# Kernel optimization log

Hardware: AMD Instinct MI355X
Metric: run time of the kernel (lower is better)

Reference implementation:

```python
import jax, jax.numpy as jnp
import numpy as np


def setup_inputs() -> dict:
    key = jax.random.key(0)
    k1, k2 = jax.random.split(key)
    x = jax.random.normal(k1, (32, 64, 64, 64), dtype=jnp.float32)
    codebook = jax.random.normal(k2, (1024, 64), dtype=jnp.float32)
    return {"x": x, "codebook": codebook}


def reference(x, codebook):
    # x: (B, D, H, W)  codebook: (K, D)
    B, D = x.shape[0], x.shape[1]
    spatial = x.shape[2:]
    flat = x.reshape(B, D, -1).transpose(0, 2, 1)  # (B, N, D)
    dot = jnp.einsum("bnd,kd->bnk", flat, codebook)
    cb_norm = jnp.sum(codebook * codebook, axis=-1)  # (K,)
    indices = jnp.argmin(cb_norm[None, None, :] - 2.0 * dot, axis=-1)  # (B, N)
    quantized = codebook[indices]  # (B, N, D) gather
    out = quantized.transpose(0, 2, 1).reshape(x.shape)
    return out, indices.reshape((B,) + spatial)
```

## Files before the change

kernel.cpp:

```cpp
#include <hip/hip_runtime.h>


typedef _Float16 f16x8 __attribute__((ext_vector_type(8)));
typedef float    f32x4 __attribute__((ext_vector_type(4)));

#define VQ_D    64
#define VQ_HW   4096
#define VQ_NPOS 131072
#define SC      2048.0f
#define EPS_Q   24
#define WS_CBN  65536
#define WS_CNQ  66560
#define WS_CBT  67584

__global__ __launch_bounds__(256)
void vq_prep(const float* __restrict__ cb, float* __restrict__ ws)
{
    const int tid = threadIdx.x;
    const int blk = blockIdx.x;
    if (blk < 64) {
        const int it   = blk * 256 + tid;
        const int ct   = it >> 8;
        const int s    = (it >> 6) & 3;
        const int lane = it & 63;
        const int ks   = s & 1, isR = s >> 1;
        const int n    = ct * 16 + (lane & 15);
        const int k0   = ks * 32 + (lane >> 4) * 8;
        const float* src = cb + n * 64 + k0;
        f16x8 o;
        #pragma unroll
        for (int j = 0; j < 8; ++j) {
            const float b = src[j];
            const _Float16 bh = (_Float16)b;
            o[j] = isR ? (_Float16)((b - (float)bh) * (-2.0f * SC))
                       : (_Float16)(-2.0f * (float)bh);
        }
        ((f16x8*)ws)[it] = o;
    } else if (blk < 128) {
        const int it = (blk - 64) * 256 + tid;
        const int k = it >> 4, j4 = it & 15;
        ((float4*)(ws + WS_CBT))[j4 * 1024 + k] = ((const float4*)cb)[it];
    } else {
        const int k = (blk - 128) * 256 + tid;
        const float4* row = (const float4*)(cb + k * 64);
        float a0 = 0.f, a1 = 0.f, a2 = 0.f, a3 = 0.f;
        #pragma unroll
        for (int j = 0; j < 16; ++j) {
            const float4 c = row[j];
            a0 = fmaf(c.x, c.x, a0); a1 = fmaf(c.y, c.y, a1);
            a2 = fmaf(c.z, c.z, a2); a3 = fmaf(c.w, c.w, a3);
        }
        const float cn = (a0 + a1) + (a2 + a3);
        ws[WS_CBN + k] = cn;
        ws[WS_CNQ + k] = cn * 2048.0f;
    }
}

#define GLOAD_LDS(GP, LP)                                                     \
    __builtin_amdgcn_global_load_lds(                                         \
        (const __attribute__((address_space(1))) unsigned int*)(GP),          \
        (__attribute__((address_space(3))) unsigned int*)(LP), 16, 0, 0)

#define STAGE2(CK, BOFF)                                                      \
    {                                                                         \
        const char* gs_ = (const char*)ws + (size_t)(CK) * 8192               \
                          + wv * 2048 + lane * 16;                            \
        char* ld_ = (char*)bbuf + (BOFF) + wv * 2048;                         \
        GLOAD_LDS(gs_, ld_);                                                  \
        GLOAD_LDS(gs_ + 1024, ld_ + 1024);                                    \
    }

#define CT_BODY(BOFF, CI, CTG)                                                \
    {                                                                         \
        const f16x8 B0 = *(const f16x8*)(lp + (BOFF) + (CI) * 4096);          \
        const f16x8 B1 = *(const f16x8*)(lp + (BOFF) + (CI) * 4096 + 1024);   \
        const f16x8 R0 = *(const f16x8*)(lp + (BOFF) + (CI) * 4096 + 2048);   \
        const f16x8 R1 = *(const f16x8*)(lp + (BOFF) + (CI) * 4096 + 3072);   \
        const float cvq = cnq_lds[(CTG) * 16 + m];                            \
        const f32x4 Ci = {cvq, cvq, cvq, cvq};                                \
        f32x4 pa[4], pb[4];                                                   \
        __builtin_amdgcn_s_setprio(1);                                        \
        _Pragma("unroll")                                                     \
        for (int tl = 0; tl < 4; ++tl) {                                      \
            pa[tl] = __builtin_amdgcn_mfma_f32_16x16x32_f16(Ak[tl][0], B0, Ci,    0,0,0); \
            pb[tl] = __builtin_amdgcn_mfma_f32_16x16x32_f16(Ak[tl][1], B1, zero4, 0,0,0); \
        }                                                                     \
        _Pragma("unroll")                                                     \
        for (int tl = 0; tl < 4; ++tl) {                                      \
            pa[tl] = __builtin_amdgcn_mfma_f32_16x16x32_f16(Ah[tl][0], R0, pa[tl], 0,0,0); \
            pb[tl] = __builtin_amdgcn_mfma_f32_16x16x32_f16(Ah[tl][1], R1, pb[tl], 0,0,0); \
        }                                                                     \
        _Pragma("unroll")                                                     \
        for (int tl = 0; tl < 4; ++tl) {                                      \
            pa[tl] = __builtin_amdgcn_mfma_f32_16x16x32_f16(Ra[tl][0], B0, pa[tl], 0,0,0); \
            pb[tl] = __builtin_amdgcn_mfma_f32_16x16x32_f16(Ra[tl][1], B1, pb[tl], 0,0,0); \
        }                                                                     \
        __builtin_amdgcn_s_setprio(0);                                        \
        const int cbase_ = (CTG) * 16 + m;                                    \
        _Pragma("unroll")                                                     \
        for (int tl = 0; tl < 4; ++tl)                                        \
            _Pragma("unroll")                                                 \
            for (int r = 0; r < 4; ++r) {                                     \
                const float q_ = pa[tl][r] + pb[tl][r];                       \
                const int k_ = ((int)q_ << 10) | cbase_;                      \
                int md_;                                                      \
                asm("v_med3_i32 %0, %1, %2, %3"                               \
                    : "=v"(md_) : "v"(k_), "v"(d1[tl][r]), "v"(d2[tl][r]));   \
                d2[tl][r] = md_;                                              \
                d1[tl][r] = (k_ < d1[tl][r]) ? k_ : d1[tl][r];                \
            }                                                                 \
    }

#define ITER_T(VMSTR, DOSTAGE, T)                                             \
    {                                                                         \
        asm volatile("s_waitcnt " VMSTR ::: "memory");                        \
        __builtin_amdgcn_s_barrier();                                         \
        if (DOSTAGE) STAGE2((T) + 3, (((T) + 3) & 3) * 8192)                  \
        const int base_ = ((T) & 3) * 8192;                                   \
        CT_BODY(base_, 0, (T) * 2)                                            \
        CT_BODY(base_, 1, (T) * 2 + 1)                                        \
    }

__global__ __launch_bounds__(256, 2)
void vq_main(const float* __restrict__ x,
             const float* __restrict__ cb,
             float* __restrict__ ws,
             float* __restrict__ out,
             float* __restrict__ idx_out)
{
    __shared__ f16x8 bbuf[4 * 512];
    __shared__ float cnq_lds[1024];
    __shared__ int   sk[256];
    __shared__ int   smg[256];
    __shared__ int   lpos[256];
    __shared__ int   lcnt;

    const int tid  = threadIdx.x;
    const int lane = tid & 63;
    const int wv   = tid >> 6;
    const int m    = lane & 15;
    const int q    = lane >> 4;

    const int p0 = blockIdx.x * 256;
    const int b  = p0 >> 12;
    const int n0 = p0 & (VQ_HW - 1);
    const float* xw = x + (size_t)b * (VQ_D * VQ_HW) + n0 + wv * 64;

    STAGE2(0, 0)
    STAGE2(1, 8192)
    STAGE2(2, 16384)

    ((float4*)cnq_lds)[tid] = ((const float4*)(ws + WS_CNQ))[tid];

    f16x8 Ah[4][2], Ak[4][2], Ra[4][2];
    #pragma unroll
    for (int tl = 0; tl < 4; ++tl)
        #pragma unroll
        for (int ks = 0; ks < 2; ++ks) {
            f16x8 h8, k8, r8;
            #pragma unroll
            for (int j = 0; j < 8; ++j) {
                const float v = xw[(size_t)(ks * 32 + q * 8 + j) * VQ_HW + tl * 16 + m];
                const _Float16 vh = (_Float16)v;
                h8[j] = vh;
                k8[j] = (_Float16)((float)vh * 2048.0f);
                r8[j] = (_Float16)((v - (float)vh) * SC);
            }
            Ah[tl][ks] = h8; Ak[tl][ks] = k8; Ra[tl][ks] = r8;
        }

    int d1[4][4], d2[4][4];
    #pragma unroll
    for (int tl = 0; tl < 4; ++tl)
        #pragma unroll
        for (int r = 0; r < 4; ++r) { d1[tl][r] = 0x7FFFFFFF; d2[tl][r] = 0x7FFFFFFF; }

    const f32x4 zero4 = {0.f, 0.f, 0.f, 0.f};
    const char* lp = (const char*)bbuf + lane * 16;

    __syncthreads();

    for (int t = 0; t < 29; ++t)
        ITER_T("vmcnt(4)", 1, t)
    ITER_T("vmcnt(4)", 0, 29)
    ITER_T("vmcnt(2)", 0, 30)
    ITER_T("vmcnt(0)", 0, 31)

    #pragma unroll
    for (int off = 1; off < 16; off <<= 1)
        #pragma unroll
        for (int tl = 0; tl < 4; ++tl)
            #pragma unroll
            for (int r = 0; r < 4; ++r) {
                const int od1 = __shfl_xor(d1[tl][r], off, 64);
                const int od2 = __shfl_xor(d2[tl][r], off, 64);
                const int mx  = (d1[tl][r] > od1) ? d1[tl][r] : od1;
                const int mn2 = (d2[tl][r] < od2) ? d2[tl][r] : od2;
                d2[tl][r] = (mx < mn2) ? mx : mn2;
                d1[tl][r] = (d1[tl][r] < od1) ? d1[tl][r] : od1;
            }

    if (m == 0) {
        #pragma unroll
        for (int tl = 0; tl < 4; ++tl)
            #pragma unroll
            for (int r = 0; r < 4; ++r) {
                const int li = wv * 64 + tl * 16 + q * 4 + r;
                sk[li]  = d1[tl][r] & 1023;
                smg[li] = (d2[tl][r] >> 10) - (d1[tl][r] >> 10);
            }
    }
    if (tid == 0) lcnt = 0;
    __syncthreads();

    const int bk = sk[tid];
    idx_out[p0 + tid] = (float)bk;
    {
        const float4* cr = (const float4*)(cb + (size_t)bk * VQ_D);
        float* ob = out + (size_t)b * (VQ_D * VQ_HW) + n0 + tid;
        #pragma unroll
        for (int d4 = 0; d4 < 16; ++d4) {
            const float4 v = cr[d4];
            ob[(size_t)(d4 * 4 + 0) * VQ_HW] = v.x;
            ob[(size_t)(d4 * 4 + 1) * VQ_HW] = v.y;
            ob[(size_t)(d4 * 4 + 2) * VQ_HW] = v.z;
            ob[(size_t)(d4 * 4 + 3) * VQ_HW] = v.w;
        }
    }
    if (smg[tid] < EPS_Q) {
        const int s_ = atomicAdd(&lcnt, 1);
        lpos[s_] = tid;
    }
    __syncthreads();

    const int nf = lcnt;
    if (nf > 0) {
        const float*  cnb  = ws + WS_CBN;
        const float4* cbT4 = (const float4*)(ws + WS_CBT);
        float* xsw = (float*)((char*)bbuf + wv * 1024);
        for (int i = wv; i < nf; i += 4) {
            const int pos = lpos[i];
            const int nn  = n0 + pos;
            xsw[lane] = x[(size_t)b * (VQ_D * VQ_HW) + (size_t)lane * VQ_HW + nn];
            float4 xr[16];
            #pragma unroll
            for (int j = 0; j < 16; ++j) xr[j] = ((const float4*)xsw)[j];

            float bd = 3.4e38f; int bk2 = 0;
            #pragma unroll 4
            for (int t = 0; t < 16; ++t) {
                const int code = t * 64 + lane;
                float a0 = 0.f, a1 = 0.f, a2 = 0.f, a3 = 0.f;
                #pragma unroll
                for (int j4 = 0; j4 < 16; ++j4) {
                    const float4 c = cbT4[j4 * 1024 + code];
                    a0 = fmaf(xr[j4].x, c.x, a0); a1 = fmaf(xr[j4].y, c.y, a1);
                    a2 = fmaf(xr[j4].z, c.z, a2); a3 = fmaf(xr[j4].w, c.w, a3);
                }
                const float dist = fmaf(-2.0f, (a0 + a1) + (a2 + a3), cnb[code]);
                if (dist < bd) { bd = dist; bk2 = code; }
            }
            #pragma unroll
            for (int off = 1; off < 64; off <<= 1) {
                const float od = __shfl_xor(bd, off, 64);
                const int   ok = __shfl_xor(bk2, off, 64);
                if (od < bd || (od == bd && ok < bk2)) { bd = od; bk2 = ok; }
            }
            out[(size_t)b * (VQ_D * VQ_HW) + (size_t)lane * VQ_HW + nn] =
                cb[(size_t)bk2 * VQ_D + lane];
            if (lane == 0) idx_out[p0 + pos] = (float)bk2;
        }
    }
}

extern "C" void kernel_launch(void* const* d_in, const int* in_sizes, int n_in,
                              void* d_out, int out_size, void* d_ws, size_t ws_size,
                              hipStream_t stream) {
    const float* x  = (const float*)d_in[0];
    const float* cb = (const float*)d_in[1];
    float* out = (float*)d_out;
    float* idx = out + (size_t)VQ_NPOS * VQ_D;
    float* ws  = (float*)d_ws;

    vq_prep<<<dim3(132), dim3(256), 0, stream>>>(cb, ws);
    vq_main<<<dim3(512), dim3(256), 0, stream>>>(x, cb, ws, out, idx);
}
```

Measured before the change: 140.9 us.

## Fuse codebook prep into main kernel with in-block f16 split conversion

Removes the separate prep kernel and workspace. Each block now loads raw fp32 codebook chunks, converts them in registers to the hi/residual f16 MFMA operands, computes the chunk norms, and writes them into a double-buffered LDS tile. The async global-to-LDS 4-stage pipeline is replaced with register-prefetch plus __syncthreads double buffering. The fallback exact path reads row-major codebook and recomputes norms itself. This saves a launch and a workspace round trip, but every block now redoes the conversion and norm work and uses full block barriers.

```diff
diff --git a/kernel.cpp b/kernel.cpp
--- a/kernel.cpp
+++ b/kernel.cpp
@@ -9,65 +9,60 @@
 #define VQ_NPOS 131072
 #define SC      2048.0f
 #define EPS_Q   24
-#define WS_CBN  65536
-#define WS_CNQ  66560
-#define WS_CBT  67584
-
-__global__ __launch_bounds__(256)
-void vq_prep(const float* __restrict__ cb, float* __restrict__ ws)
+
+__device__ __forceinline__ f16x8 pack_bh2(float4 u, float4 v)
 {
-    const int tid = threadIdx.x;
-    const int blk = blockIdx.x;
-    if (blk < 64) {
-        const int it   = blk * 256 + tid;
-        const int ct   = it >> 8;
-        const int s    = (it >> 6) & 3;
-        const int lane = it & 63;
-        const int ks   = s & 1, isR = s >> 1;
-        const int n    = ct * 16 + (lane & 15);
-        const int k0   = ks * 32 + (lane >> 4) * 8;
-        const float* src = cb + n * 64 + k0;
-        f16x8 o;
-        #pragma unroll
-        for (int j = 0; j < 8; ++j) {
-            const float b = src[j];
-            const _Float16 bh = (_Float16)b;
-            o[j] = isR ? (_Float16)((b - (float)bh) * (-2.0f * SC))
-                       : (_Float16)(-2.0f * (float)bh);
-        }
-        ((f16x8*)ws)[it] = o;
-    } else if (blk < 128) {
-        const int it = (blk - 64) * 256 + tid;
-        const int k = it >> 4, j4 = it & 15;
-        ((float4*)(ws + WS_CBT))[j4 * 1024 + k] = ((const float4*)cb)[it];
-    } else {
-        const int k = (blk - 128) * 256 + tid;
-        const float4* row = (const float4*)(cb + k * 64);
-        float a0 = 0.f, a1 = 0.f, a2 = 0.f, a3 = 0.f;
-        #pragma unroll
-        for (int j = 0; j < 16; ++j) {
-            const float4 c = row[j];
-            a0 = fmaf(c.x, c.x, a0); a1 = fmaf(c.y, c.y, a1);
-            a2 = fmaf(c.z, c.z, a2); a3 = fmaf(c.w, c.w, a3);
-        }
-        const float cn = (a0 + a1) + (a2 + a3);
-        ws[WS_CBN + k] = cn;
-        ws[WS_CNQ + k] = cn * 2048.0f;
-    }
-}
-
-#define GLOAD_LDS(GP, LP)                                                     \
-    __builtin_amdgcn_global_load_lds(                                         \
-        (const __attribute__((address_space(1))) unsigned int*)(GP),          \
-        (__attribute__((address_space(3))) unsigned int*)(LP), 16, 0, 0)
-
-#define STAGE2(CK, BOFF)                                                      \
-    {                                                                         \
-        const char* gs_ = (const char*)ws + (size_t)(CK) * 8192               \
-                          + wv * 2048 + lane * 16;                            \
-        char* ld_ = (char*)bbuf + (BOFF) + wv * 2048;                         \
-        GLOAD_LDS(gs_, ld_);                                                  \
-        GLOAD_LDS(gs_ + 1024, ld_ + 1024);                                    \
+    const float s[8] = {u.x, u.y, u.z, u.w, v.x, v.y, v.z, v.w};
+    f16x8 o;
+    #pragma unroll
+    for (int j = 0; j < 8; ++j) {
+        const _Float16 bh = (_Float16)s[j];
+        o[j] = (_Float16)(-2.0f * (float)bh);
+    }
+    return o;
+}
+
+__device__ __forceinline__ f16x8 pack_rb2k(float4 u, float4 v)
+{
+    const float s[8] = {u.x, u.y, u.z, u.w, v.x, v.y, v.z, v.w};
+    f16x8 o;
+    #pragma unroll
+    for (int j = 0; j < 8; ++j) {
+        const _Float16 bh = (_Float16)s[j];
+        o[j] = (_Float16)((s[j] - (float)bh) * (-2.0f * SC));
+    }
+    return o;
+}
+
+#define LDCHUNK(C, P0, P1, P2, P3)                                            \
+    {                                                                         \
+        const float* rw_ = cb + (size_t)(((C) * 2 + ci) * 16 + (lane & 15)) * 64 + k0x; \
+        P0 = ((const float4*)rw_)[0];       P1 = ((const float4*)rw_)[1];     \
+        P2 = ((const float4*)(rw_ + 32))[0]; P3 = ((const float4*)(rw_ + 32))[1]; \
+    }
+
+#define CONVW(P0, P1, P2, P3, SLOTB, C)                                       \
+    {                                                                         \
+        char* wb_ = (char*)bbuf + (SLOTB) + ci * 4096 + role * 2048 + lane * 16; \
+        if (role == 0) {                                                      \
+            *(f16x8*)wb_          = pack_bh2(P0, P1);                         \
+            *(f16x8*)(wb_ + 1024) = pack_bh2(P2, P3);                         \
+            float na_ = 0.f;                                                  \
+            na_ = fmaf(P0.x, P0.x, na_); na_ = fmaf(P0.y, P0.y, na_);         \
+            na_ = fmaf(P0.z, P0.z, na_); na_ = fmaf(P0.w, P0.w, na_);         \
+            na_ = fmaf(P1.x, P1.x, na_); na_ = fmaf(P1.y, P1.y, na_);         \
+            na_ = fmaf(P1.z, P1.z, na_); na_ = fmaf(P1.w, P1.w, na_);         \
+            na_ = fmaf(P2.x, P2.x, na_); na_ = fmaf(P2.y, P2.y, na_);         \
+            na_ = fmaf(P2.z, P2.z, na_); na_ = fmaf(P2.w, P2.w, na_);         \
+            na_ = fmaf(P3.x, P3.x, na_); na_ = fmaf(P3.y, P3.y, na_);         \
+            na_ = fmaf(P3.z, P3.z, na_); na_ = fmaf(P3.w, P3.w, na_);         \
+            na_ += __shfl_xor(na_, 16, 64);                                   \
+            na_ += __shfl_xor(na_, 32, 64);                                   \
+            if (lane < 16) cnq_lds[(C) * 32 + ci * 16 + lane] = na_ * 2048.0f;\
+        } else {                                                              \
+            *(f16x8*)wb_          = pack_rb2k(P0, P1);                        \
+            *(f16x8*)(wb_ + 1024) = pack_rb2k(P2, P3);                        \
+        }                                                                     \
     }
 
 #define CT_BODY(BOFF, CI, CTG)                                                \
@@ -111,12 +106,9 @@
             }                                                                 \
     }
 
-#define ITER_T(VMSTR, DOSTAGE, T)                                             \
-    {                                                                         \
-        asm volatile("s_waitcnt " VMSTR ::: "memory");                        \
-        __builtin_amdgcn_s_barrier();                                         \
-        if (DOSTAGE) STAGE2((T) + 3, (((T) + 3) & 3) * 8192)                  \
-        const int base_ = ((T) & 3) * 8192;                                   \
+#define COMPUTE(T)                                                            \
+    {                                                                         \
+        const int base_ = ((T) & 1) * 8192;                                   \
         CT_BODY(base_, 0, (T) * 2)                                            \
         CT_BODY(base_, 1, (T) * 2 + 1)                                        \
     }
@@ -124,11 +116,10 @@
 __global__ __launch_bounds__(256, 2)
 void vq_main(const float* __restrict__ x,
              const float* __restrict__ cb,
-             float* __restrict__ ws,
              float* __restrict__ out,
              float* __restrict__ idx_out)
 {
-    __shared__ f16x8 bbuf[4 * 512];
+    __shared__ f16x8 bbuf[2 * 512];
     __shared__ float cnq_lds[1024];
     __shared__ int   sk[256];
     __shared__ int   smg[256];
@@ -140,17 +131,14 @@
     const int wv   = tid >> 6;
     const int m    = lane & 15;
     const int q    = lane >> 4;
+    const int ci   = wv >> 1;
+    const int role = wv & 1;
+    const int k0x  = (lane >> 4) * 8;
 
     const int p0 = blockIdx.x * 256;
     const int b  = p0 >> 12;
     const int n0 = p0 & (VQ_HW - 1);
     const float* xw = x + (size_t)b * (VQ_D * VQ_HW) + n0 + wv * 64;
-
-    STAGE2(0, 0)
-    STAGE2(1, 8192)
-    STAGE2(2, 16384)
-
-    ((float4*)cnq_lds)[tid] = ((const float4*)(ws + WS_CNQ))[tid];
 
     f16x8 Ah[4][2], Ak[4][2], Ra[4][2];
     #pragma unroll
@@ -169,6 +157,11 @@
             Ah[tl][ks] = h8; Ak[tl][ks] = k8; Ra[tl][ks] = r8;
         }
 
+    float4 a0, a1, a2, a3, b0, b1, b2, b3;
+    LDCHUNK(0, a0, a1, a2, a3)
+    LDCHUNK(1, b0, b1, b2, b3)
+    CONVW(a0, a1, a2, a3, 0, 0)
+
     int d1[4][4], d2[4][4];
     #pragma unroll
     for (int tl = 0; tl < 4; ++tl)
@@ -180,11 +173,21 @@
 
     __syncthreads();
 
-    for (int t = 0; t < 29; ++t)
-        ITER_T("vmcnt(4)", 1, t)
-    ITER_T("vmcnt(4)", 0, 29)
-    ITER_T("vmcnt(2)", 0, 30)
-    ITER_T("vmcnt(0)", 0, 31)
+    for (int h = 0; h < 15; ++h) {
+        const int t0 = 2 * h;
+        CONVW(b0, b1, b2, b3, 8192, t0 + 1)
+        LDCHUNK(t0 + 2, a0, a1, a2, a3)
+        COMPUTE(t0)
+        __syncthreads();
+        CONVW(a0, a1, a2, a3, 0, t0 + 2)
+        LDCHUNK(t0 + 3, b0, b1, b2, b3)
+        COMPUTE(t0 + 1)
+        __syncthreads();
+    }
+    CONVW(b0, b1, b2, b3, 8192, 31)
+    COMPUTE(30)
+    __syncthreads();
+    COMPUTE(31)
 
     #pragma unroll
     for (int off = 1; off < 16; off <<= 1)
@@ -235,8 +238,6 @@
 
     const int nf = lcnt;
     if (nf > 0) {
-        const float*  cnb  = ws + WS_CBN;
-        const float4* cbT4 = (const float4*)(ws + WS_CBT);
         float* xsw = (float*)((char*)bbuf + wv * 1024);
         for (int i = wv; i < nf; i += 4) {
             const int pos = lpos[i];
@@ -250,14 +251,17 @@
             #pragma unroll 4
             for (int t = 0; t < 16; ++t) {
                 const int code = t * 64 + lane;
-                float a0 = 0.f, a1 = 0.f, a2 = 0.f, a3 = 0.f;
+                const float4* row = (const float4*)(cb + (size_t)code * VQ_D);
+                float d0 = 0.f, d1_ = 0.f, nr0 = 0.f, nr1 = 0.f;
                 #pragma unroll
                 for (int j4 = 0; j4 < 16; ++j4) {
-                    const float4 c = cbT4[j4 * 1024 + code];
-                    a0 = fmaf(xr[j4].x, c.x, a0); a1 = fmaf(xr[j4].y, c.y, a1);
-                    a2 = fmaf(xr[j4].z, c.z, a2); a3 = fmaf(xr[j4].w, c.w, a3);
+                    const float4 c = row[j4];
+                    d0  = fmaf(xr[j4].x, c.x, d0);  d1_ = fmaf(xr[j4].y, c.y, d1_);
+                    d0  = fmaf(xr[j4].z, c.z, d0);  d1_ = fmaf(xr[j4].w, c.w, d1_);
+                    nr0 = fmaf(c.x, c.x, nr0);      nr1 = fmaf(c.y, c.y, nr1);
+                    nr0 = fmaf(c.z, c.z, nr0);      nr1 = fmaf(c.w, c.w, nr1);
                 }
-                const float dist = fmaf(-2.0f, (a0 + a1) + (a2 + a3), cnb[code]);
+                const float dist = fmaf(-2.0f, d0 + d1_, nr0 + nr1);
                 if (dist < bd) { bd = dist; bk2 = code; }
             }
             #pragma unroll
@@ -280,8 +284,7 @@
     const float* cb = (const float*)d_in[1];
     float* out = (float*)d_out;
     float* idx = out + (size_t)VQ_NPOS * VQ_D;
-    float* ws  = (float*)d_ws;
-
-    vq_prep<<<dim3(132), dim3(256), 0, stream>>>(cb, ws);
-    vq_main<<<dim3(512), dim3(256), 0, stream>>>(x, cb, ws, out, idx);
-}
+    (void)d_ws; (void)ws_size;
+
+    vq_main<<<dim3(512), dim3(256), 0, stream>>>(x, cb, out, idx);
+}
```

Measured after the change: 169.0 us. +20.0%, slower.
